# Kernel optimization log

Hardware: AMD Instinct MI355X
Metric: run time of the kernel (lower is better)

Reference implementation:

```python
import jax, jax.numpy as jnp
import numpy as np

NUM_QUBITS = 4
NUM_LAYERS = 3


def _ry(state, theta, wire):
    # state: (N,2,2,2,2) real amplitudes; RY(theta) on `wire` (angle scalar or (N,))
    st = jnp.moveaxis(state, wire + 1, -1)
    c = jnp.cos(theta * 0.5)
    s = jnp.sin(theta * 0.5)
    if jnp.ndim(c) == 1:  # per-sample angle -> broadcast over remaining qubit axes
        shape = (c.shape[0],) + (1,) * (st.ndim - 2)
        c = c.reshape(shape)
        s = s.reshape(shape)
    s0, s1 = st[..., 0], st[..., 1]
    new = jnp.stack([c * s0 - s * s1, s * s0 + c * s1], axis=-1)
    return jnp.moveaxis(new, -1, wire + 1)


def _cnot(state, control, target):
    st = jnp.moveaxis(state, (control + 1, target + 1), (-2, -1))
    new = jnp.stack([st[..., 0, :], st[..., 1, ::-1]], axis=-2)
    return jnp.moveaxis(new, (-2, -1), (control + 1, target + 1))


def _circuit(angles, params):
    # angles: (N,4) input rotations; params: (L,4,1) shared variational angles
    N = angles.shape[0]
    state = jnp.zeros((N, 2, 2, 2, 2), angles.dtype).at[:, 0, 0, 0, 0].set(1.0)
    for q in range(NUM_QUBITS):
        state = _ry(state, angles[:, q], q)
    for l in range(NUM_LAYERS):
        for q in range(NUM_QUBITS):
            state = _ry(state, params[l, q, 0], q)
        for q in range(NUM_QUBITS - 1):
            state = _cnot(state, q, q + 1)
    probs = state * state  # amplitudes are real (only RY/CNOT)
    meas = []
    for w in range(NUM_QUBITS):
        axes = tuple(a for a in range(1, NUM_QUBITS + 1) if a != w + 1)
        p = probs.sum(axes)  # (N,2)
        meas.append(p[:, 0] - p[:, 1])  # <Z_w>
    return jnp.stack(meas, axis=-1)  # (N,4)


def setup_inputs() -> dict:
    key = jax.random.key(0)
    k1, k2, k3, k4, k5 = jax.random.split(key, 5)
    B = 8192
    return {
        "x": jax.random.uniform(k1, (B, 1, 28, 28), dtype=jnp.float32),
        "params": jax.random.normal(k2, (NUM_LAYERS, NUM_QUBITS, 1), dtype=jnp.float32),
        "res_w": jax.random.normal(k3, (4, 1, 1, 1), dtype=jnp.float32),
        "cls_w": jax.random.normal(k4, (10, 784), dtype=jnp.float32) * 0.03,
        "cls_b": jax.random.normal(k5, (10,), dtype=jnp.float32) * 0.03,
    }


def reference(x, params, res_w, cls_w, cls_b):
    B = x.shape[0]
    img = x.reshape(B, 28, 28)
    # extract 2x2 patches, element order (r,c),(r,c+1),(r+1,c),(r+1,c+1)
    patches = img.reshape(B, 14, 2, 14, 2).transpose(0, 1, 3, 2, 4).reshape(B, 196, 4)
    # per-patch-index min/max over batch and the 4 elements (matches patch.min()/max())
    mn = patches.min(axis=(0, 2), keepdims=True)
    mx = patches.max(axis=(0, 2), keepdims=True)
    ang = (patches - mn) / (mx - mn + 1e-8) * jnp.pi
    meas = _circuit(ang.reshape(B * 196, 4), params)  # (B*196, 4)
    out = meas.reshape(B, 196 * 4).reshape(B, 4, 14, 14)  # matches torch.cat(...).view
    # res_conv: 1x1 conv, stride 2, no bias -> strided pixel scaled per out-channel
    res = img[:, ::2, ::2][:, None, :, :] * res_w.reshape(1, 4, 1, 1)
    out = out + res
    logits = out.reshape(B, -1) @ cls_w.T + cls_b
    return jax.nn.log_softmax(logits, axis=-1)
```

## Files before the change

### kernel.cpp

```cpp
#include <hip/hip_runtime.h>
#include <math.h>

#define NP 196
#define PI_F 3.14159265358979323846f

__device__ __forceinline__ unsigned fkey(float f) {
  unsigned u = __float_as_uint(f);
  return u ^ ((unsigned)((int)u >> 31) | 0x80000000u);
}
__device__ __forceinline__ float funkey(unsigned k) {
  unsigned u = (k & 0x80000000u) ? (k ^ 0x80000000u) : ~k;
  return __uint_as_float(u);
}

__global__ void __launch_bounds__(256) precompute_kernel(
    const float* __restrict__ params, const float* __restrict__ res_w,
    const float* __restrict__ cls_w, float* __restrict__ U,
    float* __restrict__ W2) {
  const int tid = threadIdx.x;
  if (tid < 16) {
    float cp[12], sp[12];
#pragma unroll
    for (int l = 0; l < 12; ++l) __sincosf(0.5f * params[l], &sp[l], &cp[l]);
    float st[16];
#pragma unroll
    for (int i = 0; i < 16; ++i) st[i] = 0.f;
    st[tid] = 1.f;
#pragma unroll
    for (int l = 0; l < 3; ++l) {
#pragma unroll
      for (int q = 0; q < 4; ++q) {
        const float cq = cp[l * 4 + q], sq = sp[l * 4 + q];
        const int m = 8 >> q;
#pragma unroll
        for (int idx = 0; idx < 16; ++idx) {
          if (idx & m) continue;
          float v0 = st[idx], v1 = st[idx | m];
          st[idx] = cq * v0 - sq * v1;
          st[idx | m] = sq * v0 + cq * v1;
        }
      }
#pragma unroll
      for (int q = 0; q < 3; ++q) {
        const int mc = 8 >> q, mt = 4 >> q;
#pragma unroll
        for (int idx = 0; idx < 16; ++idx) {
          if ((idx & mc) && !(idx & mt)) {
            float t0 = st[idx];
            st[idx] = st[idx | mt];
            st[idx | mt] = t0;
          }
        }
      }
    }
#pragma unroll
    for (int i = 0; i < 16; ++i) U[i * 16 + tid] = st[i];
  }
  for (int t = tid; t < 10 * NP; t += 256) {
    int k = t / NP, p = t - k * NP;
    float s = 0.f;
#pragma unroll
    for (int c = 0; c < 4; ++c) s += res_w[c] * cls_w[k * 784 + c * NP + p];
    W2[t] = s;
  }
}

__global__ void __launch_bounds__(512) minmax_kernel(
    const float* __restrict__ x, unsigned* __restrict__ mn,
    unsigned* __restrict__ mx, int imgs, int B) {
  __shared__ unsigned skmin[392], skmax[392];
  const int t = threadIdx.x;
  const int img0 = blockIdx.x * imgs;
  if (t < 392) {
    const int r = t / 14, j = t - r * 14;
    const float* base = x + (size_t)img0 * 784 + r * 28 + 2 * j;
    float lmn = 3.4e38f, lmx = -3.4e38f;
    const int nimg = (img0 + imgs <= B) ? imgs : (B - img0);
#pragma unroll 4
    for (int m = 0; m < nimg; ++m) {
      float2 v = *(const float2*)(base + (size_t)m * 784);
      lmn = fminf(lmn, fminf(v.x, v.y));
      lmx = fmaxf(lmx, fmaxf(v.x, v.y));
    }
    skmin[t] = fkey(lmn);
    skmax[t] = fkey(lmx);
  }
  __syncthreads();
  if (t < NP) {
    const int i = t / 14, j = t - i * 14;
    const int f0 = (2 * i) * 14 + j, f1 = f0 + 14;
    unsigned kmn = skmin[f0] < skmin[f1] ? skmin[f0] : skmin[f1];
    unsigned kmx = skmax[f0] > skmax[f1] ? skmax[f0] : skmax[f1];
    atomicMin(&mn[t], kmn);
    atomicMax(&mx[t], kmx);
  }
}

__global__ void __launch_bounds__(256) circuit_kernel(
    const float* __restrict__ x, const unsigned* __restrict__ mnk,
    const unsigned* __restrict__ mxk, const float* __restrict__ U,
    float4* __restrict__ gmeas, int G) {
  const int g = blockIdx.x * 256 + threadIdx.x;
  if (g >= G) return;
  const int b = g / NP;
  const int p = g - b * NP;
  const int i = p / 14, j = p - i * 14;

  const float* px = x + (size_t)b * 784 + (2 * i) * 28 + 2 * j;
  const float2 r0 = *(const float2*)px;
  const float2 r1 = *(const float2*)(px + 28);

  const float mnv = funkey(mnk[p]);
  const float mxv = funkey(mxk[p]);
  const float sc = (0.5f * PI_F) / (mxv - mnv + 1e-8f);

  float cc[4], ss[4];
  __sincosf((r0.x - mnv) * sc, &ss[0], &cc[0]);
  __sincosf((r0.y - mnv) * sc, &ss[1], &cc[1]);
  __sincosf((r1.x - mnv) * sc, &ss[2], &cc[2]);
  __sincosf((r1.y - mnv) * sc, &ss[3], &cc[3]);

  float st0[16];
  {
    const float A[4] = {cc[0] * cc[1], cc[0] * ss[1], ss[0] * cc[1], ss[0] * ss[1]};
    const float Bq[4] = {cc[2] * cc[3], cc[2] * ss[3], ss[2] * cc[3], ss[2] * ss[3]};
#pragma unroll
    for (int idx = 0; idx < 16; ++idx) st0[idx] = A[idx >> 2] * Bq[idx & 3];
  }

  float z0 = 0.f, z1 = 0.f, z2 = 0.f, z3 = 0.f;
#pragma unroll
  for (int i2 = 0; i2 < 16; ++i2) {
    float f = 0.f;
#pragma unroll
    for (int jx = 0; jx < 16; ++jx) f = fmaf(U[i2 * 16 + jx], st0[jx], f);
    const float sq = f * f;
    z0 += (i2 & 8) ? -sq : sq;
    z1 += (i2 & 4) ? -sq : sq;
    z2 += (i2 & 2) ? -sq : sq;
    z3 += (i2 & 1) ? -sq : sq;
  }
  gmeas[g] = make_float4(z0, z1, z2, z3);
}

__global__ void __launch_bounds__(256) cls_kernel(
    const float* __restrict__ gmeas, const float* __restrict__ x,
    const float* __restrict__ W2, const float* __restrict__ cls_w,
    const float* __restrict__ cls_b, float* __restrict__ out, int B) {
  const int wv = (blockIdx.x * 256 + threadIdx.x) >> 6;
  const int lane = threadIdx.x & 63;
  if (wv >= B) return;
  const float* mrow = gmeas + (size_t)wv * 784;
  const float* xrow = x + (size_t)wv * 784;

  float acc[10];
#pragma unroll
  for (int k = 0; k < 10; ++k) acc[k] = 0.f;

  for (int t = lane; t < 784; t += 64) {
    const float v = mrow[t];
#pragma unroll
    for (int k = 0; k < 10; ++k) acc[k] = fmaf(v, cls_w[k * 784 + t], acc[k]);
  }
  for (int p = lane; p < NP; p += 64) {
    const int i = p / 14, j = p - i * 14;
    const float v = xrow[(2 * i) * 28 + 2 * j];
#pragma unroll
    for (int k = 0; k < 10; ++k) acc[k] = fmaf(v, W2[k * NP + p], acc[k]);
  }
#pragma unroll
  for (int k = 0; k < 10; ++k) {
    float a = acc[k];
#pragma unroll
    for (int off = 32; off > 0; off >>= 1) a += __shfl_down(a, off, 64);
    acc[k] = a;
  }
  if (lane == 0) {
    float lg[10];
#pragma unroll
    for (int k = 0; k < 10; ++k) lg[k] = acc[k] + cls_b[k];
    float m = lg[0];
#pragma unroll
    for (int k = 1; k < 10; ++k) m = fmaxf(m, lg[k]);
    float s = 0.f;
#pragma unroll
    for (int k = 0; k < 10; ++k) s += __expf(lg[k] - m);
    const float lse = m + __logf(s);
#pragma unroll
    for (int k = 0; k < 10; ++k) out[(size_t)wv * 10 + k] = lg[k] - lse;
  }
}

extern "C" void kernel_launch(void* const* d_in, const int* in_sizes, int n_in,
                              void* d_out, int out_size, void* d_ws, size_t ws_size,
                              hipStream_t stream) {
  const float* x      = (const float*)d_in[0];
  const float* params = (const float*)d_in[1];
  const float* res_w  = (const float*)d_in[2];
  const float* cls_w  = (const float*)d_in[3];
  const float* cls_b  = (const float*)d_in[4];
  float* out = (float*)d_out;
  const int B = in_sizes[0] / 784;

  unsigned* mn = (unsigned*)d_ws;
  unsigned* mx = mn + NP;
  float* U  = (float*)(mx + NP);
  float* W2 = U + 256;
  float* gmeas = W2 + 10 * NP;

  hipMemsetAsync(mn, 0xFF, NP * sizeof(unsigned), stream);
  hipMemsetAsync(mx, 0x00, NP * sizeof(unsigned), stream);

  precompute_kernel<<<1, 256, 0, stream>>>(params, res_w, cls_w, U, W2);

  const int imgs = 16;
  const int nblk1 = (B + imgs - 1) / imgs;
  minmax_kernel<<<nblk1, 512, 0, stream>>>(x, mn, mx, imgs, B);

  const int G = B * NP;
  circuit_kernel<<<(G + 255) / 256, 256, 0, stream>>>(x, mn, mx, U, (float4*)gmeas, G);

  cls_kernel<<<(B * 64 + 255) / 256, 256, 0, stream>>>(gmeas, x, W2, cls_w, cls_b, out, B);
}
```

Measured before the change: 132.4 us.

## Fuse circuit evaluation and classifier into one per-image kernel

Merges the circuit kernel and the classifier kernel into one kernel with one block per image. The measurements stay in shared memory, so the intermediate gmeas buffer is no longer written to and read back from global memory. It also replaces the two memsets with initialisation inside the precompute kernel and computes the Z expectations with a pairwise butterfly reduction. In exchange, only 196 of 256 threads do the circuit work, and the extra syncs and the cross-wave partial reduction add overhead per block.

```diff
diff --git a/kernel.cpp b/kernel.cpp
--- a/kernel.cpp
+++ b/kernel.cpp
@@ -16,8 +16,13 @@
 __global__ void __launch_bounds__(256) precompute_kernel(
     const float* __restrict__ params, const float* __restrict__ res_w,
     const float* __restrict__ cls_w, float* __restrict__ U,
-    float* __restrict__ W2) {
+    float* __restrict__ W2, unsigned* __restrict__ mn,
+    unsigned* __restrict__ mx) {
   const int tid = threadIdx.x;
+  if (tid < NP) {
+    mn[tid] = 0xFFFFFFFFu;
+    mx[tid] = 0u;
+  }
   if (tid < 16) {
     float cp[12], sp[12];
 #pragma unroll
@@ -96,89 +101,105 @@
   }
 }
 
-__global__ void __launch_bounds__(256) circuit_kernel(
+__global__ void __launch_bounds__(256) fused_kernel(
     const float* __restrict__ x, const unsigned* __restrict__ mnk,
     const unsigned* __restrict__ mxk, const float* __restrict__ U,
-    float4* __restrict__ gmeas, int G) {
-  const int g = blockIdx.x * 256 + threadIdx.x;
-  if (g >= G) return;
-  const int b = g / NP;
-  const int p = g - b * NP;
-  const int i = p / 14, j = p - i * 14;
-
-  const float* px = x + (size_t)b * 784 + (2 * i) * 28 + 2 * j;
-  const float2 r0 = *(const float2*)px;
-  const float2 r1 = *(const float2*)(px + 28);
-
-  const float mnv = funkey(mnk[p]);
-  const float mxv = funkey(mxk[p]);
-  const float sc = (0.5f * PI_F) / (mxv - mnv + 1e-8f);
-
-  float cc[4], ss[4];
-  __sincosf((r0.x - mnv) * sc, &ss[0], &cc[0]);
-  __sincosf((r0.y - mnv) * sc, &ss[1], &cc[1]);
-  __sincosf((r1.x - mnv) * sc, &ss[2], &cc[2]);
-  __sincosf((r1.y - mnv) * sc, &ss[3], &cc[3]);
-
-  float st0[16];
-  {
-    const float A[4] = {cc[0] * cc[1], cc[0] * ss[1], ss[0] * cc[1], ss[0] * ss[1]};
-    const float Bq[4] = {cc[2] * cc[3], cc[2] * ss[3], ss[2] * cc[3], ss[2] * ss[3]};
-#pragma unroll
-    for (int idx = 0; idx < 16; ++idx) st0[idx] = A[idx >> 2] * Bq[idx & 3];
-  }
-
-  float z0 = 0.f, z1 = 0.f, z2 = 0.f, z3 = 0.f;
-#pragma unroll
-  for (int i2 = 0; i2 < 16; ++i2) {
-    float f = 0.f;
-#pragma unroll
-    for (int jx = 0; jx < 16; ++jx) f = fmaf(U[i2 * 16 + jx], st0[jx], f);
-    const float sq = f * f;
-    z0 += (i2 & 8) ? -sq : sq;
-    z1 += (i2 & 4) ? -sq : sq;
-    z2 += (i2 & 2) ? -sq : sq;
-    z3 += (i2 & 1) ? -sq : sq;
-  }
-  gmeas[g] = make_float4(z0, z1, z2, z3);
-}
-
-__global__ void __launch_bounds__(256) cls_kernel(
-    const float* __restrict__ gmeas, const float* __restrict__ x,
     const float* __restrict__ W2, const float* __restrict__ cls_w,
-    const float* __restrict__ cls_b, float* __restrict__ out, int B) {
-  const int wv = (blockIdx.x * 256 + threadIdx.x) >> 6;
-  const int lane = threadIdx.x & 63;
-  if (wv >= B) return;
-  const float* mrow = gmeas + (size_t)wv * 784;
-  const float* xrow = x + (size_t)wv * 784;
+    const float* __restrict__ cls_b, float* __restrict__ out) {
+  __shared__ float lmeas[784];
+  __shared__ float respix[NP];
+  __shared__ float partial[4][10];
+
+  const int t = threadIdx.x;
+  const int b = blockIdx.x;
+
+  if (t < NP) {
+    const int p = t;
+    const int i = p / 14, j = p - i * 14;
+    const float* px = x + (size_t)b * 784 + (2 * i) * 28 + 2 * j;
+    const float2 r0 = *(const float2*)px;
+    const float2 r1 = *(const float2*)(px + 28);
+
+    const float mnv = funkey(mnk[p]);
+    const float mxv = funkey(mxk[p]);
+    const float sc = (0.5f * PI_F) / (mxv - mnv + 1e-8f);
+
+    float cc[4], ss[4];
+    __sincosf((r0.x - mnv) * sc, &ss[0], &cc[0]);
+    __sincosf((r0.y - mnv) * sc, &ss[1], &cc[1]);
+    __sincosf((r1.x - mnv) * sc, &ss[2], &cc[2]);
+    __sincosf((r1.y - mnv) * sc, &ss[3], &cc[3]);
+
+    float st0[16];
+    {
+      const float A[4] = {cc[0] * cc[1], cc[0] * ss[1], ss[0] * cc[1], ss[0] * ss[1]};
+      const float Bq[4] = {cc[2] * cc[3], cc[2] * ss[3], ss[2] * cc[3], ss[2] * ss[3]};
+#pragma unroll
+      for (int idx = 0; idx < 16; ++idx) st0[idx] = A[idx >> 2] * Bq[idx & 3];
+    }
+
+    float sq[16];
+#pragma unroll
+    for (int i2 = 0; i2 < 16; ++i2) {
+      float f = 0.f;
+#pragma unroll
+      for (int jx = 0; jx < 16; ++jx) f = fmaf(U[i2 * 16 + jx], st0[jx], f);
+      sq[i2] = f * f;
+    }
+    float a[8], z3 = 0.f;
+#pragma unroll
+    for (int k = 0; k < 8; ++k) {
+      a[k] = sq[2 * k] + sq[2 * k + 1];
+      z3 += sq[2 * k] - sq[2 * k + 1];
+    }
+    float bb[4], z2 = 0.f;
+#pragma unroll
+    for (int k = 0; k < 4; ++k) {
+      bb[k] = a[2 * k] + a[2 * k + 1];
+      z2 += a[2 * k] - a[2 * k + 1];
+    }
+    const float e0 = bb[0] + bb[1], e1 = bb[2] + bb[3];
+    const float z1 = (bb[0] - bb[1]) + (bb[2] - bb[3]);
+    const float z0 = e0 - e1;
+
+    lmeas[4 * p + 0] = z0;
+    lmeas[4 * p + 1] = z1;
+    lmeas[4 * p + 2] = z2;
+    lmeas[4 * p + 3] = z3;
+    respix[p] = r0.x;
+  }
+  __syncthreads();
 
   float acc[10];
 #pragma unroll
   for (int k = 0; k < 10; ++k) acc[k] = 0.f;
 
-  for (int t = lane; t < 784; t += 64) {
-    const float v = mrow[t];
-#pragma unroll
-    for (int k = 0; k < 10; ++k) acc[k] = fmaf(v, cls_w[k * 784 + t], acc[k]);
-  }
-  for (int p = lane; p < NP; p += 64) {
-    const int i = p / 14, j = p - i * 14;
-    const float v = xrow[(2 * i) * 28 + 2 * j];
-#pragma unroll
-    for (int k = 0; k < 10; ++k) acc[k] = fmaf(v, W2[k * NP + p], acc[k]);
-  }
+  for (int f = t; f < 784; f += 256) {
+    const float v = lmeas[f];
+#pragma unroll
+    for (int k = 0; k < 10; ++k) acc[k] = fmaf(v, cls_w[k * 784 + f], acc[k]);
+  }
+  if (t < NP) {
+    const float v = respix[t];
+#pragma unroll
+    for (int k = 0; k < 10; ++k) acc[k] = fmaf(v, W2[k * NP + t], acc[k]);
+  }
+
+  const int lane = t & 63, wv = t >> 6;
 #pragma unroll
   for (int k = 0; k < 10; ++k) {
-    float a = acc[k];
-#pragma unroll
-    for (int off = 32; off > 0; off >>= 1) a += __shfl_down(a, off, 64);
-    acc[k] = a;
-  }
-  if (lane == 0) {
+    float v = acc[k];
+#pragma unroll
+    for (int off = 32; off > 0; off >>= 1) v += __shfl_down(v, off, 64);
+    if (lane == 0) partial[wv][k] = v;
+  }
+  __syncthreads();
+
+  if (t == 0) {
     float lg[10];
 #pragma unroll
-    for (int k = 0; k < 10; ++k) lg[k] = acc[k] + cls_b[k];
+    for (int k = 0; k < 10; ++k)
+      lg[k] = partial[0][k] + partial[1][k] + partial[2][k] + partial[3][k] + cls_b[k];
     float m = lg[0];
 #pragma unroll
     for (int k = 1; k < 10; ++k) m = fmaxf(m, lg[k]);
@@ -187,7 +208,7 @@
     for (int k = 0; k < 10; ++k) s += __expf(lg[k] - m);
     const float lse = m + __logf(s);
 #pragma unroll
-    for (int k = 0; k < 10; ++k) out[(size_t)wv * 10 + k] = lg[k] - lse;
+    for (int k = 0; k < 10; ++k) out[(size_t)b * 10 + k] = lg[k] - lse;
   }
 }
 
@@ -206,19 +227,12 @@
   unsigned* mx = mn + NP;
   float* U  = (float*)(mx + NP);
   float* W2 = U + 256;
-  float* gmeas = W2 + 10 * NP;
-
-  hipMemsetAsync(mn, 0xFF, NP * sizeof(unsigned), stream);
-  hipMemsetAsync(mx, 0x00, NP * sizeof(unsigned), stream);
-
-  precompute_kernel<<<1, 256, 0, stream>>>(params, res_w, cls_w, U, W2);
+
+  precompute_kernel<<<1, 256, 0, stream>>>(params, res_w, cls_w, U, W2, mn, mx);
 
   const int imgs = 16;
   const int nblk1 = (B + imgs - 1) / imgs;
   minmax_kernel<<<nblk1, 512, 0, stream>>>(x, mn, mx, imgs, B);
 
-  const int G = B * NP;
-  circuit_kernel<<<(G + 255) / 256, 256, 0, stream>>>(x, mn, mx, U, (float4*)gmeas, G);
-
-  cls_kernel<<<(B * 64 + 255) / 256, 256, 0, stream>>>(gmeas, x, W2, cls_w, cls_b, out, B);
-}
+  fused_kernel<<<B, 256, 0, stream>>>(x, mn, mx, U, W2, cls_w, cls_b, out);
+}
```

Result: no change. 129.9 us (-1.9%).
